# Kernel tuning notes

Hardware: AMD Instinct MI355X
Metric: run time of the kernel (lower is better)

Reference implementation:

```python
import jax, jax.numpy as jnp
import numpy as np

B_TAIL = 3.0  # 'bins' arg = tail bound of the spline interval [-B, B]


def _rqs_forward(u, w, h, d):
    """Rational-quadratic spline (Durkan et al.) with linear (identity) tails.
    u: (batch, dim); w,h: (dim, K); d: (dim, K-1). Returns x (batch, dim), logdet (batch,)."""
    dim, K = w.shape
    two_b = 2.0 * B_TAIL

    widths = jax.nn.softmax(w, axis=-1) * two_b                      # (dim, K)
    cum_w = jnp.concatenate(
        [jnp.full((dim, 1), -B_TAIL, u.dtype), -B_TAIL + jnp.cumsum(widths, axis=-1)],
        axis=-1)                                                     # (dim, K+1) knot x-positions
    cum_w = cum_w.at[:, -1].set(B_TAIL)

    heights = jax.nn.softmax(h, axis=-1) * two_b                     # (dim, K)
    cum_h = jnp.concatenate(
        [jnp.full((dim, 1), -B_TAIL, u.dtype), -B_TAIL + jnp.cumsum(heights, axis=-1)],
        axis=-1)                                                     # (dim, K+1) knot y-positions
    cum_h = cum_h.at[:, -1].set(B_TAIL)

    ones = jnp.ones((dim, 1), u.dtype)
    derivs = jnp.concatenate([ones, jax.nn.softplus(d), ones], axis=-1)  # (dim, K+1)

    inside = (u >= -B_TAIL) & (u <= B_TAIL)
    uc = jnp.clip(u, -B_TAIL, B_TAIL)

    # bin search: count interior knots <= uc  -> bin index in [0, K-1]
    idx = jnp.sum(uc[:, :, None] >= cum_w[None, :, 1:-1], axis=-1)   # (batch, dim) int32

    didx = jnp.arange(dim)[None, :]                                  # (1, dim)
    xk  = cum_w[didx, idx]
    wk  = widths[didx, idx]
    yk  = cum_h[didx, idx]
    hk  = heights[didx, idx]
    dk  = derivs[didx, idx]
    dk1 = derivs[didx, idx + 1]

    delta = hk / wk                                                  # bin slope
    theta = (uc - xk) / wk
    t1m = theta * (1.0 - theta)
    denom = delta + (dk + dk1 - 2.0 * delta) * t1m
    num = hk * (delta * theta * theta + dk * t1m)
    x_in = yk + num / denom

    ld_num = delta * delta * (dk1 * theta * theta + 2.0 * delta * t1m
                              + dk * (1.0 - theta) * (1.0 - theta))
    ld_in = jnp.log(ld_num) - 2.0 * jnp.log(denom)

    x = jnp.where(inside, x_in, u)          # identity linear tails
    ld = jnp.where(inside, ld_in, 0.0)
    return x, jnp.sum(ld, axis=-1)


def setup_inputs() -> dict:
    key = jax.random.key(0)
    ku, kw, kh, kd = jax.random.split(key, 4)
    batch, dim, K = 131072, 256, 5
    u = jax.random.normal(ku, (batch, dim), dtype=jnp.float32)
    w = jax.random.uniform(kw, (dim, K), dtype=jnp.float32, minval=-0.5, maxval=0.5)
    h = jax.random.uniform(kh, (dim, K), dtype=jnp.float32, minval=-0.5, maxval=0.5)
    d = jax.random.uniform(kd, (dim, K - 1), dtype=jnp.float32, minval=-0.5, maxval=0.5)
    return {"u": u, "w": w, "h": h, "d": d}


def reference(u, w, h, d):
    return _rqs_forward(u, w, h, d)
```

## Files before the change

kernel.cpp:

```cpp
#include <hip/hip_runtime.h>
#include <math.h>

#define BATCH 131072
#define DIM 256
#define NK 5
#define BT 3.0f

__global__ __launch_bounds__(256, 5) void rqs_kernel(
    const float* __restrict__ u,
    const float* __restrict__ wp,
    const float* __restrict__ hp,
    const float* __restrict__ dp,
    float* __restrict__ x_out,
    float* __restrict__ ld_out)
{
    __shared__ float4 tabA[NK * DIM];
    __shared__ float2 tabB[NK * DIM];
    const int tid = threadIdx.x;

    {
        const int dm = tid;
        float v[NK];
        float mx, sum, scale, c;
        float wid[NK], xpos[NK], hei[NK], ypos[NK], dv[NK + 1];

        mx = -1e30f;
        #pragma unroll
        for (int k = 0; k < NK; k++) { v[k] = wp[dm * NK + k]; mx = fmaxf(mx, v[k]); }
        sum = 0.f;
        #pragma unroll
        for (int k = 0; k < NK; k++) { v[k] = expf(v[k] - mx); sum += v[k]; }
        scale = 6.0f / sum;
        c = -BT;
        #pragma unroll
        for (int k = 0; k < NK; k++) { wid[k] = v[k] * scale; xpos[k] = c; c += wid[k]; }

        mx = -1e30f;
        #pragma unroll
        for (int k = 0; k < NK; k++) { v[k] = hp[dm * NK + k]; mx = fmaxf(mx, v[k]); }
        sum = 0.f;
        #pragma unroll
        for (int k = 0; k < NK; k++) { v[k] = expf(v[k] - mx); sum += v[k]; }
        scale = 6.0f / sum;
        c = -BT;
        #pragma unroll
        for (int k = 0; k < NK; k++) { hei[k] = v[k] * scale; ypos[k] = c; c += hei[k]; }

        dv[0] = 1.0f; dv[NK] = 1.0f;
        #pragma unroll
        for (int k = 0; k < 4; k++) dv[1 + k] = log1pf(expf(dp[dm * 4 + k]));

        #pragma unroll
        for (int k = 0; k < NK; k++) {
            tabA[k * DIM + dm] = make_float4(xpos[k], 1.0f / wid[k], ypos[k], hei[k]);
            tabB[k * DIM + dm] = make_float2(dv[k], dv[k + 1]);
        }
    }
    __syncthreads();

    const int lane = tid & 63;
    const int wv   = tid >> 6;

    float kn[4][4];
    #pragma unroll
    for (int j = 0; j < 4; j++) {
        #pragma unroll
        for (int i = 0; i < 4; i++)
            kn[j][i] = tabA[(i + 1) * DIM + lane + 64 * j].x;
    }

    const int gw = (blockIdx.x << 2) | wv;
    const int nw = gridDim.x << 2;

    for (int base = gw * 2; base < BATCH; base += nw * 2) {
        float uin[2][4];
        #pragma unroll
        for (int rr = 0; rr < 2; rr++) {
            const float* up = u + (size_t)(base + rr) * DIM + lane;
            #pragma unroll
            for (int j = 0; j < 4; j++) uin[rr][j] = up[64 * j];
        }

        float ldsum[2] = {0.f, 0.f};
        #pragma unroll
        for (int rr = 0; rr < 2; rr++) {
            float xo[4];
            #pragma unroll
            for (int j = 0; j < 4; j++) {
                float uval = uin[rr][j];
                float uc = fminf(fmaxf(uval, -BT), BT);
                bool inside = (uval >= -BT) && (uval <= BT);
                int idx = 0;
                idx += (uc >= kn[j][0]);
                idx += (uc >= kn[j][1]);
                idx += (uc >= kn[j][2]);
                idx += (uc >= kn[j][3]);
                const int a = idx * DIM + lane + 64 * j;
                float4 A  = tabA[a];
                float2 Bv = tabB[a];
                float xk = A.x, iw = A.y, yk = A.z, hk = A.w;
                float dk = Bv.x, dk1 = Bv.y;

                float delta = hk * iw;
                float theta = (uc - xk) * iw;
                float omt   = 1.0f - theta;
                float t1m   = theta * omt;
                float th2   = theta * theta;
                float denom = delta + (dk + dk1 - 2.0f * delta) * t1m;
                float inv_d = __fdividef(1.0f, denom);
                float num   = hk * (delta * th2 + dk * t1m);
                float x_in  = yk + num * inv_d;
                float ldn   = (delta * delta) *
                              (dk1 * th2 + 2.0f * delta * t1m + dk * omt * omt);
                float ld    = __logf(ldn * inv_d * inv_d);

                xo[j] = inside ? x_in : uval;
                ldsum[rr] += inside ? ld : 0.0f;
            }
            float* xp = x_out + (size_t)(base + rr) * DIM + lane;
            #pragma unroll
            for (int j = 0; j < 4; j++)
                __builtin_nontemporal_store(xo[j], xp + 64 * j);
        }

        #pragma unroll
        for (int off = 32; off > 0; off >>= 1) {
            ldsum[0] += __shfl_down(ldsum[0], off, 64);
            ldsum[1] += __shfl_down(ldsum[1], off, 64);
        }
        if (lane == 0) {
            __builtin_nontemporal_store(ldsum[0], ld_out + base);
            __builtin_nontemporal_store(ldsum[1], ld_out + base + 1);
        }
    }
}

extern "C" void kernel_launch(void* const* d_in, const int* in_sizes, int n_in,
                              void* d_out, int out_size, void* d_ws, size_t ws_size,
                              hipStream_t stream) {
    const float* u  = (const float*)d_in[0];
    const float* w  = (const float*)d_in[1];
    const float* h  = (const float*)d_in[2];
    const float* dd = (const float*)d_in[3];
    float* x  = (float*)d_out;
    float* ld = x + (size_t)BATCH * DIM;
    rqs_kernel<<<2048, 256, 0, stream>>>(u, w, h, dd, x, ld);
}
```

Before: 246.5 us.

## Software-pipeline row loads, use DPP wave reduction, shrink grid

Each wave now handles four rows per iteration and prefetches the next iteration's four rows into registers while computing the current ones, so global load latency overlaps with the spline math. The shuffle-based logdet reduction is replaced with a DPP row/broadcast reduction, with the result read from lane 63. The grid drops to a fixed 1280 blocks with a matching stride. The cost is higher register pressure from the double-buffered rows under a 5-waves-per-EU launch bound, and each block now recomputes the parameter tables over more rows.

Result: no change. 251.2 us (+1.9%).

```diff
diff --git a/kernel.cpp b/kernel.cpp
--- a/kernel.cpp
+++ b/kernel.cpp
@@ -5,6 +5,17 @@
 #define DIM 256
 #define NK 5
 #define BT 3.0f
+#define NBLK 1280
+
+__device__ __forceinline__ float wave_sum_dpp(float x) {
+    x += __int_as_float(__builtin_amdgcn_update_dpp(0, __float_as_int(x), 0x111, 0xF, 0xF, true));
+    x += __int_as_float(__builtin_amdgcn_update_dpp(0, __float_as_int(x), 0x112, 0xF, 0xF, true));
+    x += __int_as_float(__builtin_amdgcn_update_dpp(0, __float_as_int(x), 0x114, 0xF, 0xF, true));
+    x += __int_as_float(__builtin_amdgcn_update_dpp(0, __float_as_int(x), 0x118, 0xF, 0xF, true));
+    x += __int_as_float(__builtin_amdgcn_update_dpp(0, __float_as_int(x), 0x142, 0xA, 0xF, true));
+    x += __int_as_float(__builtin_amdgcn_update_dpp(0, __float_as_int(x), 0x143, 0xC, 0xF, true));
+    return x;
+}
 
 __global__ __launch_bounds__(256, 5) void rqs_kernel(
     const float* __restrict__ u,
@@ -70,24 +81,36 @@
     }
 
     const int gw = (blockIdx.x << 2) | wv;
-    const int nw = gridDim.x << 2;
+    const int stride = NBLK * 4 * 4;
 
-    for (int base = gw * 2; base < BATCH; base += nw * 2) {
-        float uin[2][4];
+    float cur[4][4];
+    int row = gw * 4;
+    #pragma unroll
+    for (int rr = 0; rr < 4; rr++) {
+        const float* up = u + (size_t)(row + rr) * DIM + lane;
         #pragma unroll
-        for (int rr = 0; rr < 2; rr++) {
-            const float* up = u + (size_t)(base + rr) * DIM + lane;
+        for (int j = 0; j < 4; j++) cur[rr][j] = up[64 * j];
+    }
+
+    for (; row < BATCH; row += stride) {
+        const int nrow = row + stride;
+        float nxt[4][4];
+        if (nrow < BATCH) {
             #pragma unroll
-            for (int j = 0; j < 4; j++) uin[rr][j] = up[64 * j];
+            for (int rr = 0; rr < 4; rr++) {
+                const float* up = u + (size_t)(nrow + rr) * DIM + lane;
+                #pragma unroll
+                for (int j = 0; j < 4; j++) nxt[rr][j] = up[64 * j];
+            }
         }
 
-        float ldsum[2] = {0.f, 0.f};
         #pragma unroll
-        for (int rr = 0; rr < 2; rr++) {
+        for (int rr = 0; rr < 4; rr++) {
             float xo[4];
+            float ldsum = 0.f;
             #pragma unroll
             for (int j = 0; j < 4; j++) {
-                float uval = uin[rr][j];
+                float uval = cur[rr][j];
                 float uc = fminf(fmaxf(uval, -BT), BT);
                 bool inside = (uval >= -BT) && (uval <= BT);
                 int idx = 0;
@@ -115,22 +138,23 @@
                 float ld    = __logf(ldn * inv_d * inv_d);
 
                 xo[j] = inside ? x_in : uval;
-                ldsum[rr] += inside ? ld : 0.0f;
+                ldsum += inside ? ld : 0.0f;
             }
-            float* xp = x_out + (size_t)(base + rr) * DIM + lane;
+            float* xp = x_out + (size_t)(row + rr) * DIM + lane;
             #pragma unroll
             for (int j = 0; j < 4; j++)
                 __builtin_nontemporal_store(xo[j], xp + 64 * j);
+
+            float tot = wave_sum_dpp(ldsum);
+            if (lane == 63)
+                __builtin_nontemporal_store(tot, ld_out + row + rr);
         }
 
-        #pragma unroll
-        for (int off = 32; off > 0; off >>= 1) {
-            ldsum[0] += __shfl_down(ldsum[0], off, 64);
-            ldsum[1] += __shfl_down(ldsum[1], off, 64);
-        }
-        if (lane == 0) {
-            __builtin_nontemporal_store(ldsum[0], ld_out + base);
-            __builtin_nontemporal_store(ldsum[1], ld_out + base + 1);
+        if (nrow < BATCH) {
+            #pragma unroll
+            for (int rr = 0; rr < 4; rr++)
+                #pragma unroll
+                for (int j = 0; j < 4; j++) cur[rr][j] = nxt[rr][j];
         }
     }
 }
@@ -144,5 +168,5 @@
     const float* dd = (const float*)d_in[3];
     float* x  = (float*)d_out;
     float* ld = x + (size_t)BATCH * DIM;
-    rqs_kernel<<<2048, 256, 0, stream>>>(u, w, h, dd, x, ld);
+    rqs_kernel<<<NBLK, 256, 0, stream>>>(u, w, h, dd, x, ld);
 }
```

## Precompute per-bin spline coefficients and restructure grid into fixed-iteration 512-thread blocks

Applied to the files above, without the earlier changes.

Each block's per-bin table now holds derived spline coefficients (slope, denominator factor, numerator terms, and folded derivative terms) in two float4 entries. The per-element math becomes a short fma chain using a hardware reciprocal. The inside/outside mask for the log-det is dropped, since clamped values land on spline endpoints where the log-det is about zero. The launch changes to 1024 blocks of 512 threads with a fixed 8-iteration row loop, which halves the number of per-block table builds but leaves half the threads idle during setup and raises LDS use per block.

New measurement: 245.9 us. No clear change (-0.3%).

```diff
diff --git a/kernel.cpp b/kernel.cpp
--- a/kernel.cpp
+++ b/kernel.cpp
@@ -5,8 +5,11 @@
 #define DIM 256
 #define NK 5
 #define BT 3.0f
+#define NBLK 1024
+#define NTHR 512
+#define ITERS 8
 
-__global__ __launch_bounds__(256, 5) void rqs_kernel(
+__global__ __launch_bounds__(NTHR, 8) void rqs_kernel(
     const float* __restrict__ u,
     const float* __restrict__ wp,
     const float* __restrict__ hp,
@@ -14,15 +17,13 @@
     float* __restrict__ x_out,
     float* __restrict__ ld_out)
 {
-    __shared__ float4 tabA[NK * DIM];
-    __shared__ float2 tabB[NK * DIM];
+    __shared__ float4 tab[NK * DIM * 2];
     const int tid = threadIdx.x;
 
-    {
+    if (tid < DIM) {
         const int dm = tid;
-        float v[NK];
+        float v[NK], wid[NK], xpos[NK], hei[NK], ypos[NK], dv[NK + 1];
         float mx, sum, scale, c;
-        float wid[NK], xpos[NK], hei[NK], ypos[NK], dv[NK + 1];
 
         mx = -1e30f;
         #pragma unroll
@@ -52,8 +53,12 @@
 
         #pragma unroll
         for (int k = 0; k < NK; k++) {
-            tabA[k * DIM + dm] = make_float4(xpos[k], 1.0f / wid[k], ypos[k], hei[k]);
-            tabB[k * DIM + dm] = make_float2(dv[k], dv[k + 1]);
+            float iw  = 1.0f / wid[k];
+            float dlt = hei[k] * iw;
+            float dk  = dv[k], dk1 = dv[k + 1];
+            tab[2 * (k * DIM + dm)]     = make_float4(xpos[k], iw, dk + dk1 - 2.0f * dlt, dlt);
+            tab[2 * (k * DIM + dm) + 1] = make_float4(hei[k] * (dlt - dk), hei[k] * dk,
+                                                      ypos[k], 2.0f * (dlt - dk));
         }
     }
     __syncthreads();
@@ -63,25 +68,25 @@
 
     float kn[4][4];
     #pragma unroll
-    for (int j = 0; j < 4; j++) {
+    for (int j = 0; j < 4; j++)
         #pragma unroll
         for (int i = 0; i < 4; i++)
-            kn[j][i] = tabA[(i + 1) * DIM + lane + 64 * j].x;
-    }
+            kn[j][i] = tab[2 * ((i + 1) * DIM + lane + 64 * j)].x;
 
-    const int gw = (blockIdx.x << 2) | wv;
-    const int nw = gridDim.x << 2;
+    const int g = (blockIdx.x << 3) | wv;
 
-    for (int base = gw * 2; base < BATCH; base += nw * 2) {
+    for (int it = 0; it < ITERS; it++) {
+        const int r0 = (it << 14) | (g << 1);
+        const float* up = u + (size_t)r0 * DIM + lane;
+
         float uin[2][4];
         #pragma unroll
-        for (int rr = 0; rr < 2; rr++) {
-            const float* up = u + (size_t)(base + rr) * DIM + lane;
+        for (int rr = 0; rr < 2; rr++)
             #pragma unroll
-            for (int j = 0; j < 4; j++) uin[rr][j] = up[64 * j];
-        }
+            for (int j = 0; j < 4; j++)
+                uin[rr][j] = up[rr * DIM + 64 * j];
 
-        float ldsum[2] = {0.f, 0.f};
+        float lds[2] = {0.f, 0.f};
         #pragma unroll
         for (int rr = 0; rr < 2; rr++) {
             float xo[4];
@@ -89,35 +94,31 @@
             for (int j = 0; j < 4; j++) {
                 float uval = uin[rr][j];
                 float uc = fminf(fmaxf(uval, -BT), BT);
-                bool inside = (uval >= -BT) && (uval <= BT);
                 int idx = 0;
                 idx += (uc >= kn[j][0]);
                 idx += (uc >= kn[j][1]);
                 idx += (uc >= kn[j][2]);
                 idx += (uc >= kn[j][3]);
-                const int a = idx * DIM + lane + 64 * j;
-                float4 A  = tabA[a];
-                float2 Bv = tabB[a];
-                float xk = A.x, iw = A.y, yk = A.z, hk = A.w;
-                float dk = Bv.x, dk1 = Bv.y;
+                const int a = 2 * (idx * DIM + lane + 64 * j);
+                float4 A  = tab[a];
+                float4 Bv = tab[a + 1];
+                float xk = A.x, iw = A.y, s = A.z, dlt = A.w;
+                float p = Bv.x, q = Bv.y, yk = Bv.z, rb = Bv.w;
 
-                float delta = hk * iw;
-                float theta = (uc - xk) * iw;
-                float omt   = 1.0f - theta;
-                float t1m   = theta * omt;
-                float th2   = theta * theta;
-                float denom = delta + (dk + dk1 - 2.0f * delta) * t1m;
-                float inv_d = __fdividef(1.0f, denom);
-                float num   = hk * (delta * th2 + dk * t1m);
-                float x_in  = yk + num * inv_d;
-                float ldn   = (delta * delta) *
-                              (dk1 * th2 + 2.0f * delta * t1m + dk * omt * omt);
-                float ld    = __logf(ldn * inv_d * inv_d);
+                float th    = (uc - xk) * iw;
+                float dk    = fmaf(-0.5f, rb, dlt);
+                float r2    = dlt * dlt;
+                float denom = fmaf(fmaf(-s, th, s), th, dlt);
+                float invd  = __builtin_amdgcn_rcpf(denom);
+                float num   = th * fmaf(p, th, q);
+                float x_in  = fmaf(num, invd, yk);
+                float ldq   = fmaf(fmaf(s, th, rb), th, dk);
+                float ld    = __logf(ldq * r2 * invd * invd);
 
-                xo[j] = inside ? x_in : uval;
-                ldsum[rr] += inside ? ld : 0.0f;
+                xo[j] = (uc == uval) ? x_in : uval;
+                lds[rr] += ld;
             }
-            float* xp = x_out + (size_t)(base + rr) * DIM + lane;
+            float* xp = x_out + (size_t)(r0 + rr) * DIM + lane;
             #pragma unroll
             for (int j = 0; j < 4; j++)
                 __builtin_nontemporal_store(xo[j], xp + 64 * j);
@@ -125,12 +126,12 @@
 
         #pragma unroll
         for (int off = 32; off > 0; off >>= 1) {
-            ldsum[0] += __shfl_down(ldsum[0], off, 64);
-            ldsum[1] += __shfl_down(ldsum[1], off, 64);
+            lds[0] += __shfl_down(lds[0], off, 64);
+            lds[1] += __shfl_down(lds[1], off, 64);
         }
         if (lane == 0) {
-            __builtin_nontemporal_store(ldsum[0], ld_out + base);
-            __builtin_nontemporal_store(ldsum[1], ld_out + base + 1);
+            __builtin_nontemporal_store(lds[0], ld_out + r0);
+            __builtin_nontemporal_store(lds[1], ld_out + r0 + 1);
         }
     }
 }
@@ -144,5 +145,5 @@
     const float* dd = (const float*)d_in[3];
     float* x  = (float*)d_out;
     float* ld = x + (size_t)BATCH * DIM;
-    rqs_kernel<<<2048, 256, 0, stream>>>(u, w, h, dd, x, ld);
+    rqs_kernel<<<NBLK, NTHR, 0, stream>>>(u, w, h, dd, x, ld);
 }
```
